# Performance work log

Measured on AMD Instinct MI355X. Metric: run time of the kernel, lower is better.

The kernel has to match this reference:

```python
import jax, jax.numpy as jnp
import numpy as np

B, NH, WH, WW, C, NPOS = 64, 16, 16, 16, 64, 288
N = WH * WW


def setup_inputs() -> dict:
    key = jax.random.key(0)
    k1, k2, k3 = jax.random.split(key, 3)
    query = jax.random.normal(k1, (B, NH, N, C), dtype=jnp.float32)
    attn_logits = jax.random.normal(k2, (B, NH, N, N), dtype=jnp.float32)
    pos_emb = jax.random.normal(k3, (C, NPOS), dtype=jnp.float32) * 0.02
    return {"query": query, "attn_logits": attn_logits, "pos_emb": pos_emb,
            "Wh": WH, "Ww": WW, "npos_max": NPOS}


def _rev_cumsum(x):
    # flip -> cumsum -> flip along last axis
    return jnp.flip(jnp.cumsum(jnp.flip(x, -1), axis=-1), -1)


def reference(query, attn_logits, pos_emb, Wh, Ww, npos_max):
    B_, nH, N_, C_ = query.shape
    gates = jax.nn.sigmoid(attn_logits)                       # (B,nH,N,N)
    gates_h = gates.swapaxes(-1, -2).reshape(B_, nH, N_, Ww, Wh)
    gates_w = gates.reshape(B_, nH, N_, Wh, Ww)
    pos_h = _rev_cumsum(gates_h).reshape(B_, nH, N_, N_).swapaxes(-1, -2)
    pos_w = _rev_cumsum(gates_w).reshape(B_, nH, N_, N_)
    pos = pos_h * Ww + pos_w
    pos = jnp.minimum(pos, npos_max - 1)
    pos_floor = jnp.floor(pos)
    pos_ceil_i = jnp.ceil(pos).astype(jnp.int32)
    pos_floor_i = pos_floor.astype(jnp.int32)
    # (B,nH,N,C) @ (C,npos) -> (B,nH,N,npos)
    logits_int = jnp.einsum('bhnc,cp->bhnp', query, pos_emb)
    logits_ceil = jnp.take_along_axis(logits_int, pos_ceil_i, axis=-1)
    logits_floor = jnp.take_along_axis(logits_int, pos_floor_i, axis=-1)
    w = pos - pos_floor
    return logits_ceil * w + logits_floor * (1.0 - w)
```

## Files before the change

kernel.cpp:

```cpp
#include <hip/hip_runtime.h>


#define NPOS 288
#define NT   18
#define LTS2 292

typedef __attribute__((ext_vector_type(8))) short bf16x8;
typedef __attribute__((ext_vector_type(4))) float f32x4;

__device__ __forceinline__ unsigned short f2bf(float f) {
    unsigned u = __float_as_uint(f);
    u += 0x7FFF + ((u >> 16) & 1);
    return (unsigned short)(u >> 16);
}
__device__ __forceinline__ float bf2f(unsigned short b) {
    return __uint_as_float(((unsigned)b) << 16);
}

template <int D>
__device__ __forceinline__ float suffix_step(float v) {
    int s = __builtin_amdgcn_update_dpp(0, __float_as_int(v), 0x100 | D, 0xF, 0xF, true);
    return v + __int_as_float(s);
}

#define GLDS(gsrc, ldst) __builtin_amdgcn_global_load_lds(                      \
    (const __attribute__((address_space(1))) void*)(gsrc),                      \
    (__attribute__((address_space(3))) void*)(ldst), 16, 0, 0)

__global__ void prep_kernel(const float* __restrict__ pos_emb,
                            short* __restrict__ wsb) {
    int idx = blockIdx.x * blockDim.x + threadIdx.x;
    if (idx >= NT * 2 * 64) return;
    int l = idx & 63;
    int s = (idx >> 6) & 1;
    int t = idx >> 7;
    int col = t * 16 + (l & 15);
    int k0  = s * 32 + (l >> 4) * 8;
    short* dst = wsb + idx * 8;
    #pragma unroll
    for (int j = 0; j < 8; ++j)
        dst[j] = (short)f2bf(pos_emb[(k0 + j) * NPOS + col]);
}

__global__ __launch_bounds__(256, 8) void cope2d_kernel(
    const float* __restrict__ query,
    const float* __restrict__ attn_logits,
    const bf16x8* __restrict__ wsb8,
    float* __restrict__ out)
{
    __shared__ float smem[16 * 256];
    float* Gl = smem;
    unsigned short* Lb = (unsigned short*)smem;

    const int tid  = threadIdx.x;
    const int lane = tid & 63;
    const int wave = tid >> 6;
    const int blk  = blockIdx.x;
    const int bh   = blk >> 4;
    const int p    = blk & 15;
    const long rowbase = (long)bh * 256 + p * 16;
    const long gbase   = rowbase * 256;

    {
        const float* src = attn_logits + gbase + (long)(wave * 4) * 256 + lane * 4;
        float* dst = &Gl[(wave * 4) * 256];
        #pragma unroll
        for (int r = 0; r < 4; ++r)
            GLDS(src + r * 256, dst + r * 256);
    }

    const float* qptr = query + (rowbase + (lane & 15)) * 64 + (lane >> 4) * 8;
    bf16x8 A[2];
    #pragma unroll
    for (int s = 0; s < 2; ++s) {
        f32x4 lo = *(const f32x4*)(qptr + s * 32);
        f32x4 hi = *(const f32x4*)(qptr + s * 32 + 4);
        #pragma unroll
        for (int j = 0; j < 4; ++j) { A[s][j] = (short)f2bf(lo[j]); A[s][4 + j] = (short)f2bf(hi[j]); }
    }

    __syncthreads();

    float g[16];
    #pragma unroll
    for (int i = 0; i < 16; ++i)
        g[i] = Gl[i * 256 + tid];
    #pragma unroll
    for (int i = 0; i < 16; ++i)
        g[i] = 1.0f / (1.0f + __expf(-g[i]));

    __syncthreads();

    for (int t = wave; t < NT; t += 4) {
        f32x4 c = {0.f, 0.f, 0.f, 0.f};
        c = __builtin_amdgcn_mfma_f32_16x16x32_bf16(A[0], wsb8[(t * 2 + 0) * 64 + lane], c, 0, 0, 0);
        c = __builtin_amdgcn_mfma_f32_16x16x32_bf16(A[1], wsb8[(t * 2 + 1) * 64 + lane], c, 0, 0, 0);
        const int col = t * 16 + (lane & 15);
        const int r0  = (lane >> 4) * 4;
        #pragma unroll
        for (int r = 0; r < 4; ++r)
            Lb[(r0 + r) * LTS2 + col] = f2bf(c[r]);
    }

    __syncthreads();

    {
        float sfx[16];
        float run = 0.f;
        #pragma unroll
        for (int i = 15; i >= 0; --i) { run += g[i]; sfx[i] = run; }

        #pragma unroll
        for (int half = 0; half < 2; ++half) {
            const int i0 = half * 8;
            float w8[8]; int fi8[8];
            #pragma unroll
            for (int k = 0; k < 8; ++k) {
                const int i = i0 + k;
                float pw = suffix_step<8>(suffix_step<4>(suffix_step<2>(suffix_step<1>(g[i]))));
                float pos = fminf(sfx[i] * 16.0f + pw, 287.0f);
                float pf = floorf(pos);
                fi8[k] = (int)pf;
                w8[k]  = pos - pf;
            }
            float lf8[8], lc8[8];
            #pragma unroll
            for (int k = 0; k < 8; ++k) {
                const unsigned short* Lr = Lb + (i0 + k) * LTS2;
                lf8[k] = bf2f(Lr[fi8[k]]);
                lc8[k] = bf2f(Lr[fi8[k] + 1]);
            }
            #pragma unroll
            for (int k = 0; k < 8; ++k)
                out[gbase + (long)(i0 + k) * 256 + tid] =
                    lf8[k] + w8[k] * (lc8[k] - lf8[k]);
        }
    }
}

extern "C" void kernel_launch(void* const* d_in, const int* in_sizes, int n_in,
                              void* d_out, int out_size, void* d_ws, size_t ws_size,
                              hipStream_t stream) {
    const float* query       = (const float*)d_in[0];
    const float* attn_logits = (const float*)d_in[1];
    const float* pos_emb     = (const float*)d_in[2];
    float* outp = (float*)d_out;
    short* wsb  = (short*)d_ws;

    prep_kernel<<<9, 256, 0, stream>>>(pos_emb, wsb);
    cope2d_kernel<<<16384, 256, 0, stream>>>(query, attn_logits,
                                             (const bf16x8*)d_ws, outp);
}
```

Baseline: 140.6 us.

## Process four row-tiles per block with register prefetch of next tile's logits

Each block now handles four consecutive 16-row tiles instead of one, cutting the grid to a quarter. The next tile's attention logits and query rows are loaded into registers while the current tile's gather and store run, replacing the async global-to-LDS load. Launch bounds drop to 4 blocks per SM, trading occupancy for software pipelining. The extra register pressure and lower occupancy may leave memory latency less hidden.

```diff
diff --git a/kernel.cpp b/kernel.cpp
--- a/kernel.cpp
+++ b/kernel.cpp
@@ -23,10 +23,6 @@
     return v + __int_as_float(s);
 }
 
-#define GLDS(gsrc, ldst) __builtin_amdgcn_global_load_lds(                      \
-    (const __attribute__((address_space(1))) void*)(gsrc),                      \
-    (__attribute__((address_space(3))) void*)(ldst), 16, 0, 0)
-
 __global__ void prep_kernel(const float* __restrict__ pos_emb,
                             short* __restrict__ wsb) {
     int idx = blockIdx.x * blockDim.x + threadIdx.x;
@@ -42,83 +38,92 @@
         dst[j] = (short)f2bf(pos_emb[(k0 + j) * NPOS + col]);
 }
 
-__global__ __launch_bounds__(256, 8) void cope2d_kernel(
+__global__ __launch_bounds__(256, 4) void cope2d_kernel(
     const float* __restrict__ query,
     const float* __restrict__ attn_logits,
     const bf16x8* __restrict__ wsb8,
     float* __restrict__ out)
 {
-    __shared__ float smem[16 * 256];
-    float* Gl = smem;
-    unsigned short* Lb = (unsigned short*)smem;
+    __shared__ unsigned short Lb[16 * LTS2];
 
     const int tid  = threadIdx.x;
     const int lane = tid & 63;
     const int wave = tid >> 6;
     const int blk  = blockIdx.x;
-    const int bh   = blk >> 4;
-    const int p    = blk & 15;
-    const long rowbase = (long)bh * 256 + p * 16;
-    const long gbase   = rowbase * 256;
+    const int bh   = blk >> 2;
+    const int p0   = (blk & 3) * 4;
 
-    {
-        const float* src = attn_logits + gbase + (long)(wave * 4) * 256 + lane * 4;
-        float* dst = &Gl[(wave * 4) * 256];
-        #pragma unroll
-        for (int r = 0; r < 4; ++r)
-            GLDS(src + r * 256, dst + r * 256);
-    }
+    long rowbase = (long)bh * 256 + p0 * 16;
+    long gb      = rowbase * 256;
 
-    const float* qptr = query + (rowbase + (lane & 15)) * 64 + (lane >> 4) * 8;
-    bf16x8 A[2];
-    #pragma unroll
-    for (int s = 0; s < 2; ++s) {
-        f32x4 lo = *(const f32x4*)(qptr + s * 32);
-        f32x4 hi = *(const f32x4*)(qptr + s * 32 + 4);
-        #pragma unroll
-        for (int j = 0; j < 4; ++j) { A[s][j] = (short)f2bf(lo[j]); A[s][4 + j] = (short)f2bf(hi[j]); }
-    }
-
-    __syncthreads();
-
-    float g[16];
+    const float* qp = query + (rowbase + (lane & 15)) * 64 + (lane >> 4) * 8;
+    f32x4 q00 = *(const f32x4*)(qp);
+    f32x4 q01 = *(const f32x4*)(qp + 4);
+    f32x4 q10 = *(const f32x4*)(qp + 32);
+    f32x4 q11 = *(const f32x4*)(qp + 36);
+    float gn[16];
     #pragma unroll
     for (int i = 0; i < 16; ++i)
-        g[i] = Gl[i * 256 + tid];
-    #pragma unroll
-    for (int i = 0; i < 16; ++i)
-        g[i] = 1.0f / (1.0f + __expf(-g[i]));
+        gn[i] = attn_logits[gb + (long)i * 256 + tid];
 
-    __syncthreads();
+    for (int s = 0; s < 4; ++s) {
+        bf16x8 A0, A1;
+        #pragma unroll
+        for (int j = 0; j < 4; ++j) {
+            A0[j]     = (short)f2bf(q00[j]);
+            A0[4 + j] = (short)f2bf(q01[j]);
+            A1[j]     = (short)f2bf(q10[j]);
+            A1[4 + j] = (short)f2bf(q11[j]);
+        }
 
-    for (int t = wave; t < NT; t += 4) {
-        f32x4 c = {0.f, 0.f, 0.f, 0.f};
-        c = __builtin_amdgcn_mfma_f32_16x16x32_bf16(A[0], wsb8[(t * 2 + 0) * 64 + lane], c, 0, 0, 0);
-        c = __builtin_amdgcn_mfma_f32_16x16x32_bf16(A[1], wsb8[(t * 2 + 1) * 64 + lane], c, 0, 0, 0);
-        const int col = t * 16 + (lane & 15);
-        const int r0  = (lane >> 4) * 4;
+        if (s) __syncthreads();
+
+        for (int t = wave; t < NT; t += 4) {
+            f32x4 c = {0.f, 0.f, 0.f, 0.f};
+            c = __builtin_amdgcn_mfma_f32_16x16x32_bf16(A0, wsb8[(t * 2 + 0) * 64 + lane], c, 0, 0, 0);
+            c = __builtin_amdgcn_mfma_f32_16x16x32_bf16(A1, wsb8[(t * 2 + 1) * 64 + lane], c, 0, 0, 0);
+            const int col = t * 16 + (lane & 15);
+            const int r0  = (lane >> 4) * 4;
+            #pragma unroll
+            for (int r = 0; r < 4; ++r)
+                Lb[(r0 + r) * LTS2 + col] = f2bf(c[r]);
+        }
+
+        float g[16];
         #pragma unroll
-        for (int r = 0; r < 4; ++r)
-            Lb[(r0 + r) * LTS2 + col] = f2bf(c[r]);
-    }
+        for (int i = 0; i < 16; ++i)
+            g[i] = 1.0f / (1.0f + __expf(-gn[i]));
 
-    __syncthreads();
+        __syncthreads();
 
-    {
-        float sfx[16];
+        const long gbs = gb;
+
+        if (s < 3) {
+            rowbase += 16;
+            gb = rowbase * 256;
+            const float* qp2 = query + (rowbase + (lane & 15)) * 64 + (lane >> 4) * 8;
+            q00 = *(const f32x4*)(qp2);
+            q01 = *(const f32x4*)(qp2 + 4);
+            q10 = *(const f32x4*)(qp2 + 32);
+            q11 = *(const f32x4*)(qp2 + 36);
+            #pragma unroll
+            for (int i = 0; i < 16; ++i)
+                gn[i] = attn_logits[gb + (long)i * 256 + tid];
+        }
+
         float run = 0.f;
         #pragma unroll
-        for (int i = 15; i >= 0; --i) { run += g[i]; sfx[i] = run; }
+        for (int half = 1; half >= 0; --half) {
+            const int i0 = half * 8;
+            float r8[8];
+            #pragma unroll
+            for (int k = 7; k >= 0; --k) { run += g[i0 + k]; r8[k] = run; }
 
-        #pragma unroll
-        for (int half = 0; half < 2; ++half) {
-            const int i0 = half * 8;
             float w8[8]; int fi8[8];
             #pragma unroll
             for (int k = 0; k < 8; ++k) {
-                const int i = i0 + k;
-                float pw = suffix_step<8>(suffix_step<4>(suffix_step<2>(suffix_step<1>(g[i]))));
-                float pos = fminf(sfx[i] * 16.0f + pw, 287.0f);
+                float pw = suffix_step<8>(suffix_step<4>(suffix_step<2>(suffix_step<1>(g[i0 + k]))));
+                float pos = fminf(r8[k] * 16.0f + pw, 287.0f);
                 float pf = floorf(pos);
                 fi8[k] = (int)pf;
                 w8[k]  = pos - pf;
@@ -132,7 +137,7 @@
             }
             #pragma unroll
             for (int k = 0; k < 8; ++k)
-                out[gbase + (long)(i0 + k) * 256 + tid] =
+                out[gbs + (long)(i0 + k) * 256 + tid] =
                     lf8[k] + w8[k] * (lc8[k] - lf8[k]);
         }
     }
@@ -148,6 +153,6 @@
     short* wsb  = (short*)d_ws;
 
     prep_kernel<<<9, 256, 0, stream>>>(pos_emb, wsb);
-    cope2d_kernel<<<16384, 256, 0, stream>>>(query, attn_logits,
-                                             (const bf16x8*)d_ws, outp);
+    cope2d_kernel<<<4096, 256, 0, stream>>>(query, attn_logits,
+                                            (const bf16x8*)d_ws, outp);
 }
```

After: 139.9 us. About the same (-0.5%).
